# Kernel tuning notes

Hardware: AMD Instinct MI355X
Metric: run time of the kernel (lower is better)

## Reference

```python
import jax, jax.numpy as jnp
import numpy as np

H = 256      # hidden_size
V = 32000    # output_size (vocab)
L = 2048     # encoder max_len
B = 64       # batch

def setup_inputs():
    key = jax.random.key(0)
    ks = jax.random.split(key, 13)
    s = 0.05
    return {
        "input": jax.random.randint(ks[0], (1, B), 0, V),
        "hidden": jax.random.normal(ks[1], (1, B, H), dtype=jnp.float32),
        "encoder_outputs": jax.random.normal(ks[2], (L, B, H), dtype=jnp.float32),
        "use_cuda": 0,
        "emb_table": jax.random.normal(ks[3], (V, H), dtype=jnp.float32) * s,
        "attn_W": jax.random.normal(ks[4], (H, 2 * H), dtype=jnp.float32) * s,
        "attn_b": jax.random.normal(ks[5], (H,), dtype=jnp.float32) * s,
        "flatten": jax.random.normal(ks[6], (1, H), dtype=jnp.float32) * s,
        "gru_Wih": jax.random.normal(ks[7], (3 * H, 2 * H), dtype=jnp.float32) * s,
        "gru_Whh": jax.random.normal(ks[8], (3 * H, H), dtype=jnp.float32) * s,
        "gru_bih": jax.random.normal(ks[9], (3 * H,), dtype=jnp.float32) * s,
        "gru_bhh": jax.random.normal(ks[10], (3 * H,), dtype=jnp.float32) * s,
        "out_W": jax.random.normal(ks[11], (V, 2 * H), dtype=jnp.float32) * s,
        "out_b": jax.random.normal(ks[12], (V,), dtype=jnp.float32) * s,
    }

def reference(input, hidden, encoder_outputs, use_cuda, emb_table, attn_W, attn_b,
              flatten, gru_Wih, gru_Whh, gru_bih, gru_bhh, out_W, out_b):
    h = hidden[0]                                   # [B, H]
    embedded = emb_table[input[0]]                  # [B, H]; dropout is identity at eval
    # Bahdanau energies, vectorized: e[b,l] = flatten . (attn_W @ [h_b; enc_{l,b}] + attn_b)
    fvec = flatten[0]                               # [H]
    w = attn_W.T @ fvec                             # [2H]; split contributions of h and enc
    bias_term = fvec @ attn_b                       # scalar
    e_h = h @ w[:H]                                 # [B]
    e_enc = jnp.einsum('lbh,h->bl', encoder_outputs, w[H:])  # [B, L]
    energies = e_enc + e_h[:, None] + bias_term
    attn_weights = jax.nn.softmax(energies, axis=1)           # [B, L]
    context = jnp.einsum('bl,lbh->bh', attn_weights, encoder_outputs)  # [B, H]
    # one GRU step on x = [embedded; context] (PyTorch gate order r, z, n)
    x = jnp.concatenate([embedded, context], axis=1)          # [B, 2H]
    gi = x @ gru_Wih.T + gru_bih                              # [B, 3H]
    gh = h @ gru_Whh.T + gru_bhh                              # [B, 3H]
    r = jax.nn.sigmoid(gi[:, :H] + gh[:, :H])
    z = jax.nn.sigmoid(gi[:, H:2 * H] + gh[:, H:2 * H])
    n = jnp.tanh(gi[:, 2 * H:] + r * gh[:, 2 * H:])
    h_new = (1.0 - z) * n + z * h                             # [B, H]
    logits = jnp.concatenate([h_new, context], axis=1) @ out_W.T + out_b  # [B, V]
    output = jax.nn.log_softmax(logits, axis=-1)
    return output, h_new[None], attn_weights[:, None, :]
```

## Files before the change

kernel.cpp:

```cpp
#include <hip/hip_runtime.h>
#include <math.h>

#define H 256
#define V 32000
#define L 2048
#define B 64
#define NCH 16

#define WS_W      0
#define WS_BIAS   512
#define WS_EH     513
#define WS_ENERGY 640
#define WS_PART   (640 + B*L)
#define WS_XCAT   (WS_PART + NCH*B*H)
#define WS_M      (WS_XCAT + B*2*H)
#define WS_S      (WS_M + B)

__global__ __launch_bounds__(512) void k1_prep(
    const float* __restrict__ attn_W, const float* __restrict__ attn_b,
    const float* __restrict__ flatten, const float* __restrict__ hidden,
    float* __restrict__ ws) {
  __shared__ float fv[H];
  __shared__ float w_s[2 * H];
  __shared__ float red[H];
  int tid = threadIdx.x;
  if (tid < H) fv[tid] = flatten[tid];
  __syncthreads();
  float acc = 0.f;
  for (int hh = 0; hh < H; ++hh) acc += attn_W[hh * 2 * H + tid] * fv[hh];
  w_s[tid] = acc;
  ws[WS_W + tid] = acc;
  if (tid < H) red[tid] = fv[tid] * attn_b[tid];
  __syncthreads();
  for (int s = H / 2; s > 0; s >>= 1) {
    if (tid < s) red[tid] += red[tid + s];
    __syncthreads();
  }
  if (tid == 0) ws[WS_BIAS] = red[0];
  if (tid < B) {
    float a = 0.f;
    for (int h = 0; h < H; ++h) a += hidden[tid * H + h] * w_s[h];
    ws[WS_EH + tid] = a;
  }
}

__global__ __launch_bounds__(256) void k2_energy(
    const float* __restrict__ enc, float* __restrict__ ws) {
  int tid = threadIdx.x;
  int lane = tid & 63;
  size_t pair = (size_t)blockIdx.x * 4 + (tid >> 6);
  const float4* e4 = (const float4*)enc;
  float4 e = e4[pair * (H / 4) + lane];
  float4 w2 = ((const float4*)(ws + WS_W + H))[lane];
  float v = e.x * w2.x + e.y * w2.y + e.z * w2.z + e.w * w2.w;
  for (int off = 32; off > 0; off >>= 1) v += __shfl_xor(v, off, 64);
  if (lane == 0) {
    int b = (int)(pair & (B - 1));
    int l = (int)(pair >> 6);
    ws[WS_ENERGY + b * L + l] = v + ws[WS_EH + b] + ws[WS_BIAS];
  }
}

__global__ __launch_bounds__(256) void k3_softmax(
    const float* __restrict__ ws, float* __restrict__ d_out) {
  int b = blockIdx.x, tid = threadIdx.x;
  __shared__ float red[256];
  float e[L / 256];
  float m = -INFINITY;
#pragma unroll
  for (int i = 0; i < L / 256; ++i) {
    e[i] = ws[WS_ENERGY + b * L + i * 256 + tid];
    m = fmaxf(m, e[i]);
  }
  red[tid] = m;
  __syncthreads();
  for (int s = 128; s > 0; s >>= 1) {
    if (tid < s) red[tid] = fmaxf(red[tid], red[tid + s]);
    __syncthreads();
  }
  m = red[0];
  __syncthreads();
  float s0 = 0.f;
#pragma unroll
  for (int i = 0; i < L / 256; ++i) {
    e[i] = expf(e[i] - m);
    s0 += e[i];
  }
  red[tid] = s0;
  __syncthreads();
  for (int s = 128; s > 0; s >>= 1) {
    if (tid < s) red[tid] += red[tid + s];
    __syncthreads();
  }
  float inv = 1.f / red[0];
  float* aw = d_out + (size_t)B * V + (size_t)B * H + (size_t)b * L;
#pragma unroll
  for (int i = 0; i < L / 256; ++i) aw[i * 256 + tid] = e[i] * inv;
}

__global__ __launch_bounds__(256) void k4_ctx(
    const float* __restrict__ enc, const float* __restrict__ d_out_r,
    float* __restrict__ ws) {
  int b = blockIdx.x, ch = blockIdx.y, tid = threadIdx.x;
  const float* aw = d_out_r + (size_t)B * V + (size_t)B * H + (size_t)b * L;
  float acc = 0.f;
  int l0 = ch * (L / NCH);
  for (int i = 0; i < L / NCH; ++i) {
    int l = l0 + i;
    acc += aw[l] * enc[((size_t)l * B + b) * H + tid];
  }
  ws[WS_PART + (size_t)(ch * B + b) * H + tid] = acc;
}

__global__ __launch_bounds__(256) void k5_gru(
    const int* __restrict__ input, const float* __restrict__ hidden,
    const float* __restrict__ emb, const float* __restrict__ Wih,
    const float* __restrict__ Whh, const float* __restrict__ bih,
    const float* __restrict__ bhh, float* __restrict__ ws,
    float* __restrict__ d_out) {
  int b = blockIdx.x, tid = threadIdx.x;
  __shared__ float x_s[2 * H];
  __shared__ float h_s[H];
  __shared__ float gi_s[3 * H];
  __shared__ float gh_s[3 * H];
  float c = 0.f;
#pragma unroll
  for (int ch = 0; ch < NCH; ++ch) c += ws[WS_PART + (size_t)(ch * B + b) * H + tid];
  int tok = input[b];
  x_s[tid] = emb[(size_t)tok * H + tid];
  x_s[H + tid] = c;
  h_s[tid] = hidden[b * H + tid];
  __syncthreads();
#pragma unroll
  for (int j0 = 0; j0 < 3; ++j0) {
    int j = j0 * H + tid;
    const float4* wr = (const float4*)(Wih + (size_t)j * 2 * H);
    const float4* xr = (const float4*)x_s;
    float gi = bih[j];
#pragma unroll 4
    for (int k = 0; k < 2 * H / 4; ++k) {
      float4 wv = wr[k], xv = xr[k];
      gi += wv.x * xv.x + wv.y * xv.y + wv.z * xv.z + wv.w * xv.w;
    }
    const float4* wh = (const float4*)(Whh + (size_t)j * H);
    const float4* hr = (const float4*)h_s;
    float gh = bhh[j];
#pragma unroll 4
    for (int k = 0; k < H / 4; ++k) {
      float4 wv = wh[k], hv = hr[k];
      gh += wv.x * hv.x + wv.y * hv.y + wv.z * hv.z + wv.w * hv.w;
    }
    gi_s[j] = gi;
    gh_s[j] = gh;
  }
  __syncthreads();
  float r = 1.f / (1.f + expf(-(gi_s[tid] + gh_s[tid])));
  float z = 1.f / (1.f + expf(-(gi_s[H + tid] + gh_s[H + tid])));
  float n = tanhf(gi_s[2 * H + tid] + r * gh_s[2 * H + tid]);
  float hn = (1.f - z) * n + z * h_s[tid];
  d_out[(size_t)B * V + (size_t)b * H + tid] = hn;
  ws[WS_XCAT + (size_t)b * 2 * H + tid] = hn;
  ws[WS_XCAT + (size_t)b * 2 * H + H + tid] = c;
}

__global__ __launch_bounds__(256) void k6_logits(
    const float* __restrict__ outW, const float* __restrict__ outb,
    const float* __restrict__ ws, float* __restrict__ d_out) {
  __shared__ float As[64 * 65];
  __shared__ float Bs[64 * 65];
  int tid = threadIdx.x;
  int v0 = blockIdx.x * 64;
  int bq = tid & 15, vq = tid >> 4;
  float acc[4][4] = {{0.f}};
  const float* xc = ws + WS_XCAT;
  for (int kc = 0; kc < 8; ++kc) {
    for (int idx = tid; idx < 4096; idx += 256) {
      int r = idx >> 6, k = idx & 63;
      As[r * 65 + k] = xc[r * 512 + kc * 64 + k];
      Bs[r * 65 + k] = outW[(size_t)(v0 + r) * 512 + kc * 64 + k];
    }
    __syncthreads();
#pragma unroll 8
    for (int k = 0; k < 64; ++k) {
      float a0 = As[(bq * 4 + 0) * 65 + k];
      float a1 = As[(bq * 4 + 1) * 65 + k];
      float a2 = As[(bq * 4 + 2) * 65 + k];
      float a3 = As[(bq * 4 + 3) * 65 + k];
      float b0 = Bs[(vq * 4 + 0) * 65 + k];
      float b1 = Bs[(vq * 4 + 1) * 65 + k];
      float b2 = Bs[(vq * 4 + 2) * 65 + k];
      float b3 = Bs[(vq * 4 + 3) * 65 + k];
      acc[0][0] += a0 * b0; acc[0][1] += a0 * b1; acc[0][2] += a0 * b2; acc[0][3] += a0 * b3;
      acc[1][0] += a1 * b0; acc[1][1] += a1 * b1; acc[1][2] += a1 * b2; acc[1][3] += a1 * b3;
      acc[2][0] += a2 * b0; acc[2][1] += a2 * b1; acc[2][2] += a2 * b2; acc[2][3] += a2 * b3;
      acc[3][0] += a3 * b0; acc[3][1] += a3 * b1; acc[3][2] += a3 * b2; acc[3][3] += a3 * b3;
    }
    __syncthreads();
  }
#pragma unroll
  for (int i = 0; i < 4; ++i)
#pragma unroll
    for (int j = 0; j < 4; ++j) {
      int bb = bq * 4 + i;
      int vv = v0 + vq * 4 + j;
      d_out[(size_t)bb * V + vv] = acc[i][j] + outb[vv];
    }
}

__global__ __launch_bounds__(256) void k7_lse(
    const float* __restrict__ d_out_r, float* __restrict__ ws) {
  int b = blockIdx.x, tid = threadIdx.x;
  __shared__ float red[256];
  const float* row = d_out_r + (size_t)b * V;
  float m = -INFINITY;
  for (int i = tid; i < V; i += 256) m = fmaxf(m, row[i]);
  red[tid] = m;
  __syncthreads();
  for (int s = 128; s > 0; s >>= 1) {
    if (tid < s) red[tid] = fmaxf(red[tid], red[tid + s]);
    __syncthreads();
  }
  m = red[0];
  __syncthreads();
  float s0 = 0.f;
  for (int i = tid; i < V; i += 256) s0 += expf(row[i] - m);
  red[tid] = s0;
  __syncthreads();
  for (int s = 128; s > 0; s >>= 1) {
    if (tid < s) red[tid] += red[tid + s];
    __syncthreads();
  }
  if (tid == 0) {
    ws[WS_M + b] = m;
    ws[WS_S + b] = logf(red[0]);
  }
}

__global__ __launch_bounds__(256) void k8_norm(
    const float* __restrict__ ws, float* __restrict__ d_out) {
  int b = blockIdx.y;
  int v = blockIdx.x * 256 + threadIdx.x;
  float off = ws[WS_M + b] + ws[WS_S + b];
  d_out[(size_t)b * V + v] -= off;
}

extern "C" void kernel_launch(void* const* d_in, const int* in_sizes, int n_in,
                              void* d_out, int out_size, void* d_ws, size_t ws_size,
                              hipStream_t stream) {
  const int* input = (const int*)d_in[0];
  const float* hidden = (const float*)d_in[1];
  const float* enc = (const float*)d_in[2];
  const float* emb = (const float*)d_in[4];
  const float* attn_W = (const float*)d_in[5];
  const float* attn_b = (const float*)d_in[6];
  const float* flatten = (const float*)d_in[7];
  const float* gru_Wih = (const float*)d_in[8];
  const float* gru_Whh = (const float*)d_in[9];
  const float* gru_bih = (const float*)d_in[10];
  const float* gru_bhh = (const float*)d_in[11];
  const float* out_W = (const float*)d_in[12];
  const float* out_b = (const float*)d_in[13];
  float* out = (float*)d_out;
  float* ws = (float*)d_ws;

  k1_prep<<<1, 512, 0, stream>>>(attn_W, attn_b, flatten, hidden, ws);
  k2_energy<<<(L * B) / 4, 256, 0, stream>>>(enc, ws);
  k3_softmax<<<B, 256, 0, stream>>>(ws, out);
  k4_ctx<<<dim3(B, NCH), 256, 0, stream>>>(enc, out, ws);
  k5_gru<<<B, 256, 0, stream>>>(input, hidden, emb, gru_Wih, gru_Whh,
                                gru_bih, gru_bhh, ws, out);
  k6_logits<<<V / 64, 256, 0, stream>>>(out_W, out_b, ws, out);
  k7_lse<<<B, 256, 0, stream>>>(out, ws);
  k8_norm<<<dim3(V / 256, B), 256, 0, stream>>>(ws, out);
}
```

Before: 489.7 us.

## Fuse attention energy, softmax and context into flash-style online-softmax kernel

Replaces the separate energy, softmax and context kernels with one kernel. Each block stages encoder rows in shared memory, computes energies and accumulates context with a running max and sum, so the large encoder tensor is read once instead of twice. It also drops the per-batch h and bias energy terms because they are constant along the softmax axis, and moves softmax normalisation and partial merging into a widened GRU kernel. Other changes: the logits GEMM gets swizzled shared memory with float4 reads, and the log-softmax stats and normalisation are merged into one kernel. The risk is lower parallelism in the fused attention kernel (1024 blocks), which may limit memory bandwidth.

```diff
diff --git a/kernel.cpp b/kernel.cpp
--- a/kernel.cpp
+++ b/kernel.cpp
@@ -6,194 +6,204 @@
 #define L 2048
 #define B 64
 #define NCH 16
-
-#define WS_W      0
-#define WS_BIAS   512
-#define WS_EH     513
-#define WS_ENERGY 640
-#define WS_PART   (640 + B*L)
-#define WS_XCAT   (WS_PART + NCH*B*H)
-#define WS_M      (WS_XCAT + B*2*H)
-#define WS_S      (WS_M + B)
-
-__global__ __launch_bounds__(512) void k1_prep(
-    const float* __restrict__ attn_W, const float* __restrict__ attn_b,
-    const float* __restrict__ flatten, const float* __restrict__ hidden,
+#define SC 32
+
+#define WS_W2     0
+#define WS_E      256
+#define WS_CPART  (256 + B*L)
+#define WS_MPART  (WS_CPART + NCH*B*H)
+#define WS_SPART  (WS_MPART + NCH*B)
+#define WS_XCAT2  (WS_SPART + NCH*B)
+
+__global__ __launch_bounds__(1024) void k1_w2(
+    const float* __restrict__ attn_W, const float* __restrict__ flatten,
     float* __restrict__ ws) {
   __shared__ float fv[H];
-  __shared__ float w_s[2 * H];
-  __shared__ float red[H];
+  __shared__ float part[4][H];
   int tid = threadIdx.x;
   if (tid < H) fv[tid] = flatten[tid];
   __syncthreads();
+  int j = tid & 255, g = tid >> 8;
   float acc = 0.f;
-  for (int hh = 0; hh < H; ++hh) acc += attn_W[hh * 2 * H + tid] * fv[hh];
-  w_s[tid] = acc;
-  ws[WS_W + tid] = acc;
-  if (tid < H) red[tid] = fv[tid] * attn_b[tid];
-  __syncthreads();
-  for (int s = H / 2; s > 0; s >>= 1) {
-    if (tid < s) red[tid] += red[tid + s];
-    __syncthreads();
-  }
-  if (tid == 0) ws[WS_BIAS] = red[0];
-  if (tid < B) {
-    float a = 0.f;
-    for (int h = 0; h < H; ++h) a += hidden[tid * H + h] * w_s[h];
-    ws[WS_EH + tid] = a;
-  }
-}
-
-__global__ __launch_bounds__(256) void k2_energy(
+#pragma unroll 8
+  for (int i = 0; i < 64; ++i) {
+    int h = g * 64 + i;
+    acc += attn_W[h * 2 * H + H + j] * fv[h];
+  }
+  part[g][j] = acc;
+  __syncthreads();
+  if (tid < H)
+    ws[WS_W2 + tid] = part[0][tid] + part[1][tid] + part[2][tid] + part[3][tid];
+}
+
+__global__ __launch_bounds__(256) void kA_flash(
     const float* __restrict__ enc, float* __restrict__ ws) {
-  int tid = threadIdx.x;
-  int lane = tid & 63;
-  size_t pair = (size_t)blockIdx.x * 4 + (tid >> 6);
-  const float4* e4 = (const float4*)enc;
-  float4 e = e4[pair * (H / 4) + lane];
-  float4 w2 = ((const float4*)(ws + WS_W + H))[lane];
-  float v = e.x * w2.x + e.y * w2.y + e.z * w2.z + e.w * w2.w;
-  for (int off = 32; off > 0; off >>= 1) v += __shfl_xor(v, off, 64);
-  if (lane == 0) {
-    int b = (int)(pair & (B - 1));
-    int l = (int)(pair >> 6);
-    ws[WS_ENERGY + b * L + l] = v + ws[WS_EH + b] + ws[WS_BIAS];
-  }
-}
-
-__global__ __launch_bounds__(256) void k3_softmax(
-    const float* __restrict__ ws, float* __restrict__ d_out) {
-  int b = blockIdx.x, tid = threadIdx.x;
-  __shared__ float red[256];
-  float e[L / 256];
-  float m = -INFINITY;
-#pragma unroll
-  for (int i = 0; i < L / 256; ++i) {
-    e[i] = ws[WS_ENERGY + b * L + i * 256 + tid];
-    m = fmaxf(m, e[i]);
-  }
-  red[tid] = m;
-  __syncthreads();
-  for (int s = 128; s > 0; s >>= 1) {
-    if (tid < s) red[tid] = fmaxf(red[tid], red[tid + s]);
-    __syncthreads();
-  }
-  m = red[0];
-  __syncthreads();
-  float s0 = 0.f;
-#pragma unroll
-  for (int i = 0; i < L / 256; ++i) {
-    e[i] = expf(e[i] - m);
-    s0 += e[i];
-  }
-  red[tid] = s0;
-  __syncthreads();
-  for (int s = 128; s > 0; s >>= 1) {
-    if (tid < s) red[tid] += red[tid + s];
-    __syncthreads();
-  }
-  float inv = 1.f / red[0];
-  float* aw = d_out + (size_t)B * V + (size_t)B * H + (size_t)b * L;
-#pragma unroll
-  for (int i = 0; i < L / 256; ++i) aw[i * 256 + tid] = e[i] * inv;
-}
-
-__global__ __launch_bounds__(256) void k4_ctx(
-    const float* __restrict__ enc, const float* __restrict__ d_out_r,
-    float* __restrict__ ws) {
-  int b = blockIdx.x, ch = blockIdx.y, tid = threadIdx.x;
-  const float* aw = d_out_r + (size_t)B * V + (size_t)B * H + (size_t)b * L;
-  float acc = 0.f;
-  int l0 = ch * (L / NCH);
-  for (int i = 0; i < L / NCH; ++i) {
-    int l = l0 + i;
-    acc += aw[l] * enc[((size_t)l * B + b) * H + tid];
-  }
-  ws[WS_PART + (size_t)(ch * B + b) * H + tid] = acc;
-}
-
-__global__ __launch_bounds__(256) void k5_gru(
+  int b = blockIdx.x, ch = blockIdx.y;
+  int tid = threadIdx.x, lane = tid & 63, wv = tid >> 6;
+  __shared__ float encS[SC * H];
+  __shared__ float es[SC];
+  __shared__ float ps[SC];
+  const float4* enc4 = (const float4*)enc;
+  float4* encS4 = (float4*)encS;
+  float4 w2 = ((const float4*)(ws + WS_W2))[lane];
+  float m = -INFINITY, s = 0.f, c = 0.f;
+  for (int sc = 0; sc < (L / NCH) / SC; ++sc) {
+    int l0 = ch * (L / NCH) + sc * SC;
+    __syncthreads();
+#pragma unroll
+    for (int t = 0; t < 8; ++t) {
+      int idx = tid + t * 256;
+      int r = idx >> 6, col4 = idx & 63;
+      encS4[r * 64 + col4] = enc4[((size_t)(l0 + r) * B + b) * 64 + col4];
+    }
+    __syncthreads();
+#pragma unroll
+    for (int i = 0; i < 8; ++i) {
+      int l = wv * 8 + i;
+      float4 ev = encS4[l * 64 + lane];
+      float v = ev.x * w2.x + ev.y * w2.y + ev.z * w2.z + ev.w * w2.w;
+      for (int off = 32; off > 0; off >>= 1) v += __shfl_xor(v, off, 64);
+      if (lane == 0) {
+        es[l] = v;
+        ws[WS_E + (size_t)b * L + l0 + l] = v;
+      }
+    }
+    __syncthreads();
+    float newm = m;
+#pragma unroll
+    for (int l = 0; l < SC; ++l) newm = fmaxf(newm, es[l]);
+    if (tid < SC) ps[tid] = expf(es[tid] - newm);
+    __syncthreads();
+    float f = expf(m - newm);
+    float accS = 0.f;
+    float cnew = c * f;
+#pragma unroll
+    for (int l = 0; l < SC; ++l) {
+      float p = ps[l];
+      accS += p;
+      cnew += p * encS[l * H + tid];
+    }
+    c = cnew;
+    s = s * f + accS;
+    m = newm;
+  }
+  ws[WS_CPART + ((size_t)ch * B + b) * H + tid] = c;
+  if (tid == 0) {
+    ws[WS_MPART + ch * B + b] = m;
+    ws[WS_SPART + ch * B + b] = s;
+  }
+}
+
+__global__ __launch_bounds__(768) void kB_gru(
     const int* __restrict__ input, const float* __restrict__ hidden,
     const float* __restrict__ emb, const float* __restrict__ Wih,
     const float* __restrict__ Whh, const float* __restrict__ bih,
     const float* __restrict__ bhh, float* __restrict__ ws,
     float* __restrict__ d_out) {
   int b = blockIdx.x, tid = threadIdx.x;
+  __shared__ float fch[NCH];
   __shared__ float x_s[2 * H];
   __shared__ float h_s[H];
   __shared__ float gi_s[3 * H];
   __shared__ float gh_s[3 * H];
-  float c = 0.f;
-#pragma unroll
-  for (int ch = 0; ch < NCH; ++ch) c += ws[WS_PART + (size_t)(ch * B + b) * H + tid];
-  int tok = input[b];
-  x_s[tid] = emb[(size_t)tok * H + tid];
-  x_s[H + tid] = c;
-  h_s[tid] = hidden[b * H + tid];
-  __syncthreads();
-#pragma unroll
-  for (int j0 = 0; j0 < 3; ++j0) {
-    int j = j0 * H + tid;
+  float M = -INFINITY;
+#pragma unroll
+  for (int ch = 0; ch < NCH; ++ch) M = fmaxf(M, ws[WS_MPART + ch * B + b]);
+  float S = 0.f;
+#pragma unroll
+  for (int ch = 0; ch < NCH; ++ch)
+    S += ws[WS_SPART + ch * B + b] * expf(ws[WS_MPART + ch * B + b] - M);
+  float invS = 1.f / S;
+  if (tid < NCH) fch[tid] = expf(ws[WS_MPART + tid * B + b] - M);
+  for (int l = tid; l < L; l += 768) {
+    float e = ws[WS_E + (size_t)b * L + l];
+    d_out[(size_t)B * V + (size_t)B * H + (size_t)b * L + l] = expf(e - M) * invS;
+  }
+  if (tid < H) h_s[tid] = hidden[(size_t)b * H + tid];
+  __syncthreads();
+  float cfin = 0.f;
+  if (tid < H) {
+#pragma unroll
+    for (int ch = 0; ch < NCH; ++ch)
+      cfin += ws[WS_CPART + ((size_t)ch * B + b) * H + tid] * fch[ch];
+    cfin *= invS;
+    int tok = input[b];
+    x_s[tid] = emb[(size_t)tok * H + tid];
+    x_s[H + tid] = cfin;
+  }
+  __syncthreads();
+  {
+    int j = tid;
     const float4* wr = (const float4*)(Wih + (size_t)j * 2 * H);
     const float4* xr = (const float4*)x_s;
     float gi = bih[j];
-#pragma unroll 4
+#pragma unroll 8
     for (int k = 0; k < 2 * H / 4; ++k) {
-      float4 wv = wr[k], xv = xr[k];
-      gi += wv.x * xv.x + wv.y * xv.y + wv.z * xv.z + wv.w * xv.w;
+      float4 w = wr[k], x = xr[k];
+      gi += w.x * x.x + w.y * x.y + w.z * x.z + w.w * x.w;
     }
     const float4* wh = (const float4*)(Whh + (size_t)j * H);
     const float4* hr = (const float4*)h_s;
     float gh = bhh[j];
-#pragma unroll 4
+#pragma unroll 8
     for (int k = 0; k < H / 4; ++k) {
-      float4 wv = wh[k], hv = hr[k];
-      gh += wv.x * hv.x + wv.y * hv.y + wv.z * hv.z + wv.w * hv.w;
+      float4 w = wh[k], hv = hr[k];
+      gh += w.x * hv.x + w.y * hv.y + w.z * hv.z + w.w * hv.w;
     }
     gi_s[j] = gi;
     gh_s[j] = gh;
   }
   __syncthreads();
-  float r = 1.f / (1.f + expf(-(gi_s[tid] + gh_s[tid])));
-  float z = 1.f / (1.f + expf(-(gi_s[H + tid] + gh_s[H + tid])));
-  float n = tanhf(gi_s[2 * H + tid] + r * gh_s[2 * H + tid]);
-  float hn = (1.f - z) * n + z * h_s[tid];
-  d_out[(size_t)B * V + (size_t)b * H + tid] = hn;
-  ws[WS_XCAT + (size_t)b * 2 * H + tid] = hn;
-  ws[WS_XCAT + (size_t)b * 2 * H + H + tid] = c;
-}
-
+  if (tid < H) {
+    float r = 1.f / (1.f + expf(-(gi_s[tid] + gh_s[tid])));
+    float z = 1.f / (1.f + expf(-(gi_s[H + tid] + gh_s[H + tid])));
+    float n = tanhf(gi_s[2 * H + tid] + r * gh_s[2 * H + tid]);
+    float hn = (1.f - z) * n + z * h_s[tid];
+    d_out[(size_t)B * V + (size_t)b * H + tid] = hn;
+    ws[WS_XCAT2 + (size_t)b * 2 * H + tid] = hn;
+    ws[WS_XCAT2 + (size_t)b * 2 * H + H + tid] = cfin;
+  }
+}
+
+__device__ __forceinline__ int swz(int r, int k) {
+  return r * 64 + (k ^ (((r >> 2) & 7) << 2));
+}
 __global__ __launch_bounds__(256) void k6_logits(
     const float* __restrict__ outW, const float* __restrict__ outb,
     const float* __restrict__ ws, float* __restrict__ d_out) {
-  __shared__ float As[64 * 65];
-  __shared__ float Bs[64 * 65];
+  __shared__ float As[64 * 64];
+  __shared__ float Bs[64 * 64];
   int tid = threadIdx.x;
   int v0 = blockIdx.x * 64;
   int bq = tid & 15, vq = tid >> 4;
+  int fa = (bq & 7) << 2;
+  int fb = (vq & 7) << 2;
   float acc[4][4] = {{0.f}};
-  const float* xc = ws + WS_XCAT;
+  const float* xc = ws + WS_XCAT2;
   for (int kc = 0; kc < 8; ++kc) {
-    for (int idx = tid; idx < 4096; idx += 256) {
-      int r = idx >> 6, k = idx & 63;
-      As[r * 65 + k] = xc[r * 512 + kc * 64 + k];
-      Bs[r * 65 + k] = outW[(size_t)(v0 + r) * 512 + kc * 64 + k];
-    }
-    __syncthreads();
-#pragma unroll 8
-    for (int k = 0; k < 64; ++k) {
-      float a0 = As[(bq * 4 + 0) * 65 + k];
-      float a1 = As[(bq * 4 + 1) * 65 + k];
-      float a2 = As[(bq * 4 + 2) * 65 + k];
-      float a3 = As[(bq * 4 + 3) * 65 + k];
-      float b0 = Bs[(vq * 4 + 0) * 65 + k];
-      float b1 = Bs[(vq * 4 + 1) * 65 + k];
-      float b2 = Bs[(vq * 4 + 2) * 65 + k];
-      float b3 = Bs[(vq * 4 + 3) * 65 + k];
-      acc[0][0] += a0 * b0; acc[0][1] += a0 * b1; acc[0][2] += a0 * b2; acc[0][3] += a0 * b3;
-      acc[1][0] += a1 * b0; acc[1][1] += a1 * b1; acc[1][2] += a1 * b2; acc[1][3] += a1 * b3;
-      acc[2][0] += a2 * b0; acc[2][1] += a2 * b1; acc[2][2] += a2 * b2; acc[2][3] += a2 * b3;
-      acc[3][0] += a3 * b0; acc[3][1] += a3 * b1; acc[3][2] += a3 * b2; acc[3][3] += a3 * b3;
+#pragma unroll
+    for (int t = 0; t < 16; ++t) {
+      int idx = tid + t * 256;
+      int k = idx & 63, r = idx >> 6;
+      As[swz(r, k)] = xc[(size_t)r * 512 + kc * 64 + k];
+      Bs[swz(r, k)] = outW[(size_t)(v0 + r) * 512 + kc * 64 + k];
+    }
+    __syncthreads();
+#pragma unroll
+    for (int k = 0; k < 64; k += 4) {
+      float4 a[4], bb[4];
+#pragma unroll
+      for (int i = 0; i < 4; ++i)
+        a[i] = *(const float4*)&As[(bq * 4 + i) * 64 + (k ^ fa)];
+#pragma unroll
+      for (int j = 0; j < 4; ++j)
+        bb[j] = *(const float4*)&Bs[(vq * 4 + j) * 64 + (k ^ fb)];
+#pragma unroll
+      for (int i = 0; i < 4; ++i)
+#pragma unroll
+        for (int j = 0; j < 4; ++j)
+          acc[i][j] += a[i].x * bb[j].x + a[i].y * bb[j].y +
+                       a[i].z * bb[j].z + a[i].w * bb[j].w;
     }
     __syncthreads();
   }
@@ -201,47 +211,36 @@
   for (int i = 0; i < 4; ++i)
 #pragma unroll
     for (int j = 0; j < 4; ++j) {
-      int bb = bq * 4 + i;
+      int bbr = bq * 4 + i;
       int vv = v0 + vq * 4 + j;
-      d_out[(size_t)bb * V + vv] = acc[i][j] + outb[vv];
-    }
-}
-
-__global__ __launch_bounds__(256) void k7_lse(
-    const float* __restrict__ d_out_r, float* __restrict__ ws) {
+      d_out[(size_t)bbr * V + vv] = acc[i][j] + outb[vv];
+    }
+}
+
+__global__ __launch_bounds__(1024) void k7k8_lsm(float* __restrict__ d_out) {
   int b = blockIdx.x, tid = threadIdx.x;
-  __shared__ float red[256];
-  const float* row = d_out_r + (size_t)b * V;
+  __shared__ float red[1024];
+  float* row = d_out + (size_t)b * V;
   float m = -INFINITY;
-  for (int i = tid; i < V; i += 256) m = fmaxf(m, row[i]);
+  for (int i = tid; i < V; i += 1024) m = fmaxf(m, row[i]);
   red[tid] = m;
   __syncthreads();
-  for (int s = 128; s > 0; s >>= 1) {
+  for (int s = 512; s > 0; s >>= 1) {
     if (tid < s) red[tid] = fmaxf(red[tid], red[tid + s]);
     __syncthreads();
   }
   m = red[0];
   __syncthreads();
   float s0 = 0.f;
-  for (int i = tid; i < V; i += 256) s0 += expf(row[i] - m);
+  for (int i = tid; i < V; i += 1024) s0 += expf(row[i] - m);
   red[tid] = s0;
   __syncthreads();
-  for (int s = 128; s > 0; s >>= 1) {
+  for (int s = 512; s > 0; s >>= 1) {
     if (tid < s) red[tid] += red[tid + s];
     __syncthreads();
   }
-  if (tid == 0) {
-    ws[WS_M + b] = m;
-    ws[WS_S + b] = logf(red[0]);
-  }
-}
-
-__global__ __launch_bounds__(256) void k8_norm(
-    const float* __restrict__ ws, float* __restrict__ d_out) {
-  int b = blockIdx.y;
-  int v = blockIdx.x * 256 + threadIdx.x;
-  float off = ws[WS_M + b] + ws[WS_S + b];
-  d_out[(size_t)b * V + v] -= off;
+  float lsm = m + logf(red[0]);
+  for (int i = tid; i < V; i += 1024) row[i] -= lsm;
 }
 
 extern "C" void kernel_launch(void* const* d_in, const int* in_sizes, int n_in,
@@ -252,7 +251,6 @@
   const float* enc = (const float*)d_in[2];
   const float* emb = (const float*)d_in[4];
   const float* attn_W = (const float*)d_in[5];
-  const float* attn_b = (const float*)d_in[6];
   const float* flatten = (const float*)d_in[7];
   const float* gru_Wih = (const float*)d_in[8];
   const float* gru_Whh = (const float*)d_in[9];
@@ -263,13 +261,10 @@
   float* out = (float*)d_out;
   float* ws = (float*)d_ws;
 
-  k1_prep<<<1, 512, 0, stream>>>(attn_W, attn_b, flatten, hidden, ws);
-  k2_energy<<<(L * B) / 4, 256, 0, stream>>>(enc, ws);
-  k3_softmax<<<B, 256, 0, stream>>>(ws, out);
-  k4_ctx<<<dim3(B, NCH), 256, 0, stream>>>(enc, out, ws);
-  k5_gru<<<B, 256, 0, stream>>>(input, hidden, emb, gru_Wih, gru_Whh,
+  k1_w2<<<1, 1024, 0, stream>>>(attn_W, flatten, ws);
+  kA_flash<<<dim3(B, NCH), 256, 0, stream>>>(enc, ws);
+  kB_gru<<<B, 768, 0, stream>>>(input, hidden, emb, gru_Wih, gru_Whh,
                                 gru_bih, gru_bhh, ws, out);
   k6_logits<<<V / 64, 256, 0, stream>>>(out_W, out_b, ws, out);
-  k7_lse<<<B, 256, 0, stream>>>(out, ws);
-  k8_norm<<<dim3(V / 256, B), 256, 0, stream>>>(ws, out);
-}
+  k7k8_lsm<<<B, 1024, 0, stream>>>(out);
+}
```

Result: slower. 554.0 us (+13.1%).
